# Kernel optimization log

Hardware: AMD Instinct MI355X
Metric: run time of the kernel (lower is better)

The kernel has to match this reference:

```python
import jax, jax.numpy as jnp
import numpy as np

# Config (scaled-down DeepSeek-style MoE)
B, S, H = 4, 1024, 1024       # batch, seq, hidden_size
I = 512                        # intermediate_size per expert
E = 64                         # num_routed_experts
K = 8                          # top-k
C = 1024
NS = 1                         # num_shared_experts


def setup_inputs() -> dict:
    key = jax.random.key(0)
    ks = jax.random.split(key, 8)
    def w(k, shape, fan_in):
        return jax.random.normal(k, shape, jnp.float32) / np.float32(np.sqrt(fan_in))
    return {
        "hidden_states": jax.random.normal(ks[0], (B, S, H), jnp.float32),
        "gate_w":    w(ks[1], (E, H), H),            # nn.Linear(H, E).weight
        "shared_wg": w(ks[2], (I * NS, H), H),       # shared SwiGLU gate_proj
        "shared_wu": w(ks[3], (I * NS, H), H),       # shared SwiGLU up_proj
        "shared_wd": w(ks[4], (H, I * NS), I * NS),  # shared SwiGLU down_proj
        "expert_wg": w(ks[5], (E, I, H), H),         # routed gate_proj, stacked
        "expert_wu": w(ks[6], (E, I, H), H),         # routed up_proj, stacked
        "expert_wd": w(ks[7], (E, H, I), I),         # routed down_proj, stacked
    }


def reference(hidden_states, gate_w, shared_wg, shared_wu, shared_wd,
              expert_wg, expert_wu, expert_wd):
    b, s, h = hidden_states.shape
    x = hidden_states.reshape(-1, h)                     # [T, H]
    T = x.shape[0]

    # ---- shared expert (SwiGLU) ----
    shared = (jax.nn.silu(x @ shared_wg.T) * (x @ shared_wu.T)) @ shared_wd.T

    # ---- gating: sigmoid scores, top-k, normalize by sum ----
    scores = jax.nn.sigmoid(x @ gate_w.T)                # [T, E]
    topw, topi = jax.lax.top_k(scores, K)                # [T, K]
    topw = topw / topw.sum(-1, keepdims=True)

    # ---- dispatch: position of each (token, slot) within its expert ----
    e_flat = topi.reshape(-1)                            # [N] expert id per routed row
    N = e_flat.shape[0]
    order = jnp.argsort(e_flat)                          # rows sorted by expert id
    sorted_e = e_flat[order]
    seg_start = jnp.searchsorted(sorted_e, jnp.arange(E))
    pos_sorted = (jnp.arange(N) - seg_start[sorted_e]).astype(jnp.int32)
    pos = jnp.zeros(N, jnp.int32).at[order].set(pos_sorted)  # slot within expert buffer

    tok = jnp.repeat(jnp.arange(T), K)                   # token id per routed row
    xin = x[tok]                                         # [N, H]

    # scatter tokens into per-expert buffers [E, C, H]
    buf = jnp.zeros((E, C, h), x.dtype).at[e_flat, pos].set(xin, mode='drop')

    # per-expert SwiGLU via batched GEMMs (grouped-GEMM equivalent)
    g = jax.nn.silu(jnp.einsum('ech,eih->eci', buf, expert_wg))
    u = jnp.einsum('ech,eih->eci', buf, expert_wu)
    out_buf = jnp.einsum('eci,ehi->ech', g * u, expert_wd)  # [E, C, H]

    # gather back and combine with normalized top-k weights
    rows = out_buf[e_flat, pos]                          # [N, H]
    routed = (rows.reshape(T, K, h) * topw[..., None]).sum(1)

    return (shared + routed).reshape(b, s, h)
```

## Files before the change

### kernel.cpp

```cpp
#include <hip/hip_runtime.h>
#include <hip/hip_bf16.h>

#define TOK 4096
#define HD 1024
#define ID 512
#define NE 64
#define TK 8
#define CAP 1024
#define NROUTE 32768
#define NCHUNK 128

typedef __attribute__((ext_vector_type(4))) float f32x4;
typedef __attribute__((ext_vector_type(8))) short s16x8;
typedef __attribute__((ext_vector_type(2))) __bf16 bf16x2;

__device__ __forceinline__ ushort f2bf(float f){
  uint u = __builtin_bit_cast(uint, f);
  u += 0x7fffu + ((u >> 16) & 1u);
  return (ushort)(u >> 16);
}
__device__ __forceinline__ float bf2f(ushort b){
  uint u = ((uint)b) << 16;
  return __builtin_bit_cast(float, u);
}
__device__ __forceinline__ uint2 f4_to_bf4(float4 v){
  bf16x2 p0; p0[0] = (__bf16)v.x; p0[1] = (__bf16)v.y;
  bf16x2 p1; p1[0] = (__bf16)v.z; p1[1] = (__bf16)v.w;
  uint2 r; r.x = __builtin_bit_cast(uint, p0); r.y = __builtin_bit_cast(uint, p1);
  return r;
}
__device__ __forceinline__ short bfs(float f){
  __bf16 h = (__bf16)f;
  return __builtin_bit_cast(short, h);
}
__device__ __forceinline__ s16x8 pack8(f32x4 a, f32x4 b){
  s16x8 r;
  r[0]=bfs(a[0]); r[1]=bfs(a[1]); r[2]=bfs(a[2]); r[3]=bfs(a[3]);
  r[4]=bfs(b[0]); r[5]=bfs(b[1]); r[6]=bfs(b[2]); r[7]=bfs(b[3]);
  return r;
}
__device__ __forceinline__ void gld16(void* lds, const void* g){
  __builtin_amdgcn_global_load_lds((const __attribute__((address_space(1))) unsigned int*)g,
                                   (__attribute__((address_space(3))) unsigned int*)lds, 16, 0, 0);
}

__global__ __launch_bounds__(256)
void cvtX_kernel(const float* __restrict__ X, ushort* __restrict__ Xbf){
  size_t i = ((size_t)blockIdx.x*256 + threadIdx.x) * 8;
  float4 a = *(const float4*)(X + i);
  float4 b = *(const float4*)(X + i + 4);
  uint2 lo = f4_to_bf4(a), hi = f4_to_bf4(b);
  uint4 o; o.x = lo.x; o.y = lo.y; o.z = hi.x; o.w = hi.y;
  *(uint4*)(Xbf + i) = o;
}

__global__ __launch_bounds__(256)
void gating_kernel(const float* __restrict__ X, const float* __restrict__ GW,
                   int* __restrict__ topi, float* __restrict__ topw)
{
  __shared__ float xt[16][68];
  __shared__ float gt[64][68];
  __shared__ double ds[16][72];
  const int tid = threadIdx.x;
  const int tbase = blockIdx.x * 16;
  const int t = tid & 15, e0 = (tid >> 4) * 4;
  double acc[4] = {0.0, 0.0, 0.0, 0.0};
  for (int hc=0; hc<HD; hc+=64){
    { int r = tid >> 4, c4 = (tid & 15) * 4;
      *(float4*)&xt[r][c4] = *(const float4*)(X + (size_t)(tbase+r)*HD + hc + c4); }
    #pragma unroll
    for (int it=0; it<4; ++it){
      int idx = it*256 + tid;
      int r = idx >> 4, c4 = (idx & 15) * 4;
      *(float4*)&gt[r][c4] = *(const float4*)(GW + (size_t)r*HD + hc + c4);
    }
    __syncthreads();
    #pragma unroll
    for (int k4=0; k4<16; ++k4){
      float4 xv = *(const float4*)&xt[t][k4*4];
      #pragma unroll
      for (int j=0;j<4;++j){
        float4 gv = *(const float4*)&gt[e0+j][k4*4];
        acc[j] += (double)xv.x*(double)gv.x + (double)xv.y*(double)gv.y
                + (double)xv.z*(double)gv.z + (double)xv.w*(double)gv.w;
      }
    }
    __syncthreads();
  }
  #pragma unroll
  for (int j=0;j<4;++j) ds[t][e0+j] = acc[j];
  __syncthreads();
  if (tid < 16){
    int tt = tid;
    int idxs[8]; double vals[8]; double sum = 0.0;
    #pragma unroll
    for (int k=0;k<8;++k){
      double best = -1e300; int bi = 0;
      for (int e=0;e<NE;++e){ double v = ds[tt][e]; if (v > best){ best = v; bi = e; } }
      ds[tt][bi] = -1e300;
      double w = 1.0 / (1.0 + exp(-best));
      idxs[k] = bi; vals[k] = w; sum += w;
    }
    double inv = 1.0 / sum;
    #pragma unroll
    for (int k=0;k<8;++k){
      topi[(size_t)(tbase+tt)*TK + k] = idxs[k];
      topw[(size_t)(tbase+tt)*TK + k] = (float)(vals[k]*inv);
    }
  }
}

__global__ __launch_bounds__(256)
void hist_kernel(const int* __restrict__ topi, int* __restrict__ ccnt){
  __shared__ int h[NE];
  const int tid = threadIdx.x;
  if (tid < NE) h[tid] = 0;
  __syncthreads();
  atomicAdd(&h[topi[blockIdx.x*256 + tid]], 1);
  __syncthreads();
  if (tid < NE) ccnt[blockIdx.x*NE + tid] = h[tid];
}

__global__ __launch_bounds__(64)
void scan_kernel(const int* __restrict__ ccnt, int* __restrict__ cbase,
                 int* __restrict__ cntC, int* __restrict__ ebase){
  const int e = threadIdx.x;
  int run = 0;
  for (int c=0;c<NCHUNK;++c){ cbase[c*NE+e] = run; run += ccnt[c*NE+e]; }
  cntC[e] = run < CAP ? run : CAP;
  __syncthreads();
  if (e == 0){
    int s = 0;
    for (int i=0;i<NE;++i){ ebase[i] = s; s += cntC[i]; }
    ebase[NE] = s;
  }
}

__global__ __launch_bounds__(64)
void assign_kernel(const int* __restrict__ topi, const int* __restrict__ cbase,
                   int* __restrict__ pos, int* __restrict__ rowlist){
  __shared__ int es[256];
  const int tid = threadIdx.x;
  const int c = blockIdx.x;
  for (int i=tid;i<256;i+=64) es[i] = topi[c*256+i];
  __syncthreads();
  const int e = tid;
  int cntr = cbase[c*NE+e];
  for (int j=0;j<256;++j){
    if (es[j] == e){
      int n = c*256+j;
      pos[n] = cntr;
      if (cntr < CAP) rowlist[e*CAP + cntr] = n;
      ++cntr;
    }
  }
}

template<bool SHARED>
__global__ __launch_bounds__(256,2)
void gateup_kernel(const ushort* __restrict__ Xbf, const float* __restrict__ WG,
                   const float* __restrict__ WU, const int* __restrict__ rowlist,
                   const int* __restrict__ cntC, const int* __restrict__ ebase,
                   ushort* __restrict__ interm)
{
  int e, mt, nt, cnt, outbase;
  if (SHARED){
    nt = blockIdx.x & 7; mt = blockIdx.x >> 3; e = 0; cnt = TOK; outbase = mt*128;
  } else {
    int x = blockIdx.x & 7; int rem = blockIdx.x >> 3;
    nt = rem & 7; mt = (rem >> 3) & 7; e = ((rem >> 6) << 3) | x;
    cnt = cntC[e];
    if (mt*128 >= cnt) return;
    outbase = ebase[e] + mt*128;
  }
  const size_t wof = SHARED ? 0 : (size_t)e*ID*HD;
  const float* wg = WG + wof + (size_t)nt*64*HD;
  const float* wu = WU + wof + (size_t)nt*64*HD;

  __shared__ ushort aL[64*128];
  __shared__ float  bF[128*64];
  __shared__ int tokb[128];

  const int tid = threadIdx.x;
  if (tid < 128){
    int tokv;
    if (SHARED) tokv = mt*128 + tid;
    else tokv = (mt*128 + tid < cnt) ? (rowlist[e*CAP + mt*128 + tid] >> 3) : 0;
    tokb[tid] = tokv;
  }
  __syncthreads();

  const int w = tid >> 6, l = tid & 63;
  const int wm = w >> 1, wn = w & 1;
  const int fr = l & 15, fko = (l >> 4) * 8;

  const ushort* aSrc[4];
  #pragma unroll
  for (int j=0;j<4;++j){
    int f = j*256 + tid;
    int L = f >> 4, s = f & 15;
    int g = s ^ (L & 15);
    int row = 2*L + (g >> 3);
    aSrc[j] = Xbf + (size_t)tokb[row]*HD + (g & 7)*8;
  }
  const float* bSrc[8];
  #pragma unroll
  for (int j=0;j<8;++j){
    int f = j*256 + tid;
    int R = f >> 4, s = f & 15;
    int g = s ^ (R & 15);
    const float* base = (j < 4) ? wg : wu;
    int r2 = (j < 4) ? R : (R - 64);
    bSrc[j] = base + (size_t)r2*HD + g*4;
  }

  f32x4 accg[4][2], accu[4][2];
  #pragma unroll
  for (int i=0;i<4;++i)
    #pragma unroll
    for (int j=0;j<2;++j){ accg[i][j] = (f32x4)0.0f; accu[i][j] = (f32x4)0.0f; }

  auto stage = [&](int kc){
    #pragma unroll
    for (int j=0;j<4;++j) gld16(aL + (size_t)(j*256 + w*64)*8, aSrc[j] + kc);
    #pragma unroll
    for (int j=0;j<8;++j) gld16(bF + (size_t)(j*256 + w*64)*4, bSrc[j] + kc);
  };

  stage(0);
  for (int kc=0; kc<HD; kc+=64){
    __syncthreads();
    #pragma unroll
    for (int ks=0; ks<2; ++ks){
      s16x8 a[4];
      #pragma unroll
      for (int mb=0; mb<4; ++mb){
        int r = wm*64 + mb*16 + fr;
        int agl = ks*4 + (fko >> 3);
        int g = ((r & 1) << 3) | agl;
        int L = r >> 1;
        int gs = g ^ (L & 15);
        a[mb] = *(const s16x8*)&aL[L*128 + gs*8];
      }
      #pragma unroll
      for (int cg=0; cg<2; ++cg){
        int Rg = wn*32 + cg*16 + fr;
        int gl0 = ks*8 + (fko >> 2);
        int x0 = Rg*64 + ((gl0 ^ (Rg & 15)) * 4);
        int x1 = Rg*64 + (((gl0+1) ^ (Rg & 15)) * 4);
        s16x8 bg = pack8(*(const f32x4*)&bF[x0], *(const f32x4*)&bF[x1]);
        int Ru = 64 + wn*32 + cg*16 + fr;
        int y0 = Ru*64 + ((gl0 ^ (Ru & 15)) * 4);
        int y1 = Ru*64 + (((gl0+1) ^ (Ru & 15)) * 4);
        s16x8 bu = pack8(*(const f32x4*)&bF[y0], *(const f32x4*)&bF[y1]);
        #pragma unroll
        for (int mb=0; mb<4; ++mb){
          accg[mb][cg] = __builtin_amdgcn_mfma_f32_16x16x32_bf16(a[mb], bg, accg[mb][cg], 0, 0, 0);
          accu[mb][cg] = __builtin_amdgcn_mfma_f32_16x16x32_bf16(a[mb], bu, accu[mb][cg], 0, 0, 0);
        }
      }
    }
    __syncthreads();
    if (kc + 64 < HD) stage(kc + 64);
  }

  const int rq = (l >> 4) * 4;
  #pragma unroll
  for (int mb=0; mb<4; ++mb){
    #pragma unroll
    for (int q=0; q<4; ++q){
      int rloc = wm*64 + mb*16 + rq + q;
      if (!SHARED && mt*128 + rloc >= cnt) continue;
      size_t orow = (size_t)(outbase + rloc);
      #pragma unroll
      for (int cg=0; cg<2; ++cg){
        float g = accg[mb][cg][q], u = accu[mb][cg][q];
        float sv = g / (1.0f + __expf(-g)) * u;
        interm[orow*ID + (size_t)(nt*64 + wn*32 + cg*16 + fr)] = f2bf(sv);
      }
    }
  }
}

template<bool SHARED>
__global__ __launch_bounds__(256,2)
void down_kernel(const ushort* __restrict__ interm, const float* __restrict__ WD,
                 const int* __restrict__ cntC, const int* __restrict__ ebase,
                 ushort* __restrict__ out_rows, float* __restrict__ outf)
{
  int e, mt, nt, cnt, abase;
  if (SHARED){
    nt = blockIdx.x & 7; mt = blockIdx.x >> 3; e = 0; cnt = TOK; abase = mt*128;
  } else {
    int x = blockIdx.x & 7; int rem = blockIdx.x >> 3;
    nt = rem & 7; mt = (rem >> 3) & 7; e = ((rem >> 6) << 3) | x;
    cnt = cntC[e];
    if (mt*128 >= cnt) return;
    abase = ebase[e] + mt*128;
  }
  const ushort* A = interm + (size_t)abase*ID;
  const float* wd = WD + (SHARED ? (size_t)0 : (size_t)e*HD*ID) + (size_t)nt*128*ID;

  __shared__ ushort aL[64*128];
  __shared__ float  bF[128*64];

  const int tid = threadIdx.x;
  const int w = tid >> 6, l = tid & 63;
  const int wm = w >> 1, wn = w & 1;
  const int fr = l & 15, fko = (l >> 4) * 8;

  const ushort* aSrc[4];
  #pragma unroll
  for (int j=0;j<4;++j){
    int f = j*256 + tid;
    int L = f >> 4, s = f & 15;
    int g = s ^ (L & 15);
    int row = 2*L + (g >> 3);
    aSrc[j] = A + (size_t)row*ID + (g & 7)*8;
  }
  const float* bSrc[8];
  #pragma unroll
  for (int j=0;j<8;++j){
    int f = j*256 + tid;
    int R = f >> 4, s = f & 15;
    int g = s ^ (R & 15);
    bSrc[j] = wd + (size_t)R*ID + g*4;
  }

  f32x4 acc[4][4];
  #pragma unroll
  for (int i=0;i<4;++i)
    #pragma unroll
    for (int j=0;j<4;++j) acc[i][j] = (f32x4)0.0f;

  auto stage = [&](int kc){
    #pragma unroll
    for (int j=0;j<4;++j) gld16(aL + (size_t)(j*256 + w*64)*8, aSrc[j] + kc);
    #pragma unroll
    for (int j=0;j<8;++j) gld16(bF + (size_t)(j*256 + w*64)*4, bSrc[j] + kc);
  };

  stage(0);
  for (int kc=0; kc<ID; kc+=64){
    __syncthreads();
    #pragma unroll
    for (int ks=0; ks<2; ++ks){
      s16x8 a[4];
      #pragma unroll
      for (int mb=0; mb<4; ++mb){
        int r = wm*64 + mb*16 + fr;
        int agl = ks*4 + (fko >> 3);
        int g = ((r & 1) << 3) | agl;
        int L = r >> 1;
        int gs = g ^ (L & 15);
        a[mb] = *(const s16x8*)&aL[L*128 + gs*8];
      }
      #pragma unroll
      for (int cg=0; cg<4; ++cg){
        int R = wn*64 + cg*16 + fr;
        int gl0 = ks*8 + (fko >> 2);
        int x0 = R*64 + ((gl0 ^ (R & 15)) * 4);
        int x1 = R*64 + (((gl0+1) ^ (R & 15)) * 4);
        s16x8 bd = pack8(*(const f32x4*)&bF[x0], *(const f32x4*)&bF[x1]);
        #pragma unroll
        for (int mb=0; mb<4; ++mb){
          acc[mb][cg] = __builtin_amdgcn_mfma_f32_16x16x32_bf16(a[mb], bd, acc[mb][cg], 0, 0, 0);
        }
      }
    }
    __syncthreads();
    if (kc + 64 < ID) stage(kc + 64);
  }

  const int rq = (l >> 4) * 4;
  #pragma unroll
  for (int mb=0; mb<4; ++mb){
    #pragma unroll
    for (int q=0; q<4; ++q){
      int rloc = wm*64 + mb*16 + rq + q;
      if (!SHARED && mt*128 + rloc >= cnt) continue;
      #pragma unroll
      for (int cg=0; cg<4; ++cg){
        float v = acc[mb][cg][q];
        int colg = nt*128 + wn*64 + cg*16 + fr;
        if (SHARED) outf[(size_t)(mt*128 + rloc)*HD + colg] = v;
        else        out_rows[(size_t)(abase + rloc)*HD + colg] = f2bf(v);
      }
    }
  }
}

__global__ __launch_bounds__(256)
void combine_kernel(const int* __restrict__ topi, const float* __restrict__ topw,
                    const int* __restrict__ pos, const int* __restrict__ ebase,
                    const ushort* __restrict__ out_rows, float* __restrict__ out)
{
  const int t = blockIdx.x;
  const int tid = threadIdx.x;
  __shared__ int rws[TK];
  __shared__ float wts[TK];
  if (tid < TK){
    int e = topi[(size_t)t*TK + tid];
    int p = pos[(size_t)t*TK + tid];
    rws[tid] = (p < CAP) ? (ebase[e] + p) : -1;
    wts[tid] = topw[(size_t)t*TK + tid];
  }
  __syncthreads();
  const int h0 = tid * 4;
  float4 acc = *(float4*)(out + (size_t)t*HD + h0);
  #pragma unroll
  for (int k=0;k<TK;++k){
    int r = rws[k];
    if (r < 0) continue;
    ushort4 v = *(const ushort4*)(out_rows + (size_t)r*HD + h0);
    float wk = wts[k];
    acc.x += wk*bf2f(v.x); acc.y += wk*bf2f(v.y);
    acc.z += wk*bf2f(v.z); acc.w += wk*bf2f(v.w);
  }
  *(float4*)(out + (size_t)t*HD + h0) = acc;
}

extern "C" void kernel_launch(void* const* d_in, const int* in_sizes, int n_in,
                              void* d_out, int out_size, void* d_ws, size_t ws_size,
                              hipStream_t stream)
{
  (void)in_sizes; (void)n_in; (void)out_size; (void)ws_size;
  const float* X   = (const float*)d_in[0];
  const float* GW  = (const float*)d_in[1];
  const float* SWG = (const float*)d_in[2];
  const float* SWU = (const float*)d_in[3];
  const float* SWD = (const float*)d_in[4];
  const float* EWG = (const float*)d_in[5];
  const float* EWU = (const float*)d_in[6];
  const float* EWD = (const float*)d_in[7];
  float* OUT = (float*)d_out;

  char* p = (char*)d_ws;
  int*    topi    = (int*)p;      p += (size_t)NROUTE*4;
  float*  topw    = (float*)p;    p += (size_t)NROUTE*4;
  int*    pos     = (int*)p;      p += (size_t)NROUTE*4;
  int*    ccnt    = (int*)p;      p += (size_t)NCHUNK*NE*4;
  int*    cbase   = (int*)p;      p += (size_t)NCHUNK*NE*4;
  int*    cntC    = (int*)p;      p += 256;
  int*    ebase   = (int*)p;      p += 512;
  int*    rowlist = (int*)p;      p += (size_t)NE*CAP*4;
  ushort* Xbf     = (ushort*)p;   p += (size_t)TOK*HD*2;
  ushort* interm_r= (ushort*)p;   p += (size_t)(NROUTE+128)*ID*2;
  ushort* interm_s= (ushort*)p;   p += (size_t)TOK*ID*2;
  ushort* out_rows= (ushort*)p;   p += (size_t)NROUTE*HD*2;

  cvtX_kernel<<<TOK*HD/8/256, 256, 0, stream>>>(X, Xbf);
  gating_kernel<<<256, 256, 0, stream>>>(X, GW, topi, topw);
  hist_kernel<<<NCHUNK, 256, 0, stream>>>(topi, ccnt);
  scan_kernel<<<1, 64, 0, stream>>>(ccnt, cbase, cntC, ebase);
  assign_kernel<<<NCHUNK, 64, 0, stream>>>(topi, cbase, pos, rowlist);

  gateup_kernel<false><<<4096, 256, 0, stream>>>(Xbf, EWG, EWU, rowlist, cntC, ebase, interm_r);
  gateup_kernel<true ><<<256,  256, 0, stream>>>(Xbf, SWG, SWU, nullptr, nullptr, nullptr, interm_s);
  down_kernel<false><<<4096, 256, 0, stream>>>(interm_r, EWD, cntC, ebase, out_rows, nullptr);
  down_kernel<true ><<<256,  256, 0, stream>>>(interm_s, SWD, nullptr, nullptr, nullptr, OUT);

  combine_kernel<<<TOK, 256, 0, stream>>>(topi, topw, pos, ebase, out_rows, OUT);
}
```

Baseline: 391.6 us.

## Use 32x32x16 MFMA with 256-row tiles and fragment-ordered LDS layout

Both expert GEMM kernels switch from 16x16x32 to 32x32x16 bf16 MFMA. The M tile grows from 128 to 256 rows per block, which halves the grid and the number of times the fp32 weights are re-read per expert. The LDS layout is reorganized so each lane's MFMA fragment is stored contiguously, replacing the XOR swizzle. The risks are more wasted work on partially filled 256-row expert tiles, fewer blocks in flight, higher accumulator register pressure, and possible LDS bank conflicts on the staging writes.

Result: slower. 577.5 us (+47.5%).

```diff
diff --git a/kernel.cpp b/kernel.cpp
--- a/kernel.cpp
+++ b/kernel.cpp
@@ -11,6 +11,7 @@
 #define NCHUNK 128
 
 typedef __attribute__((ext_vector_type(4))) float f32x4;
+typedef __attribute__((ext_vector_type(16))) float f32x16;
 typedef __attribute__((ext_vector_type(8))) short s16x8;
 typedef __attribute__((ext_vector_type(2))) __bf16 bf16x2;
 
@@ -165,64 +166,59 @@
 {
   int e, mt, nt, cnt, outbase;
   if (SHARED){
-    nt = blockIdx.x & 7; mt = blockIdx.x >> 3; e = 0; cnt = TOK; outbase = mt*128;
+    nt = blockIdx.x & 7; mt = blockIdx.x >> 3; e = 0; cnt = TOK; outbase = mt*256;
   } else {
     int x = blockIdx.x & 7; int rem = blockIdx.x >> 3;
-    nt = rem & 7; mt = (rem >> 3) & 7; e = ((rem >> 6) << 3) | x;
+    nt = rem & 7; mt = (rem >> 3) & 3; e = ((rem >> 5) << 3) | x;
     cnt = cntC[e];
-    if (mt*128 >= cnt) return;
-    outbase = ebase[e] + mt*128;
+    if (mt*256 >= cnt) return;
+    outbase = ebase[e] + mt*256;
   }
   const size_t wof = SHARED ? 0 : (size_t)e*ID*HD;
   const float* wg = WG + wof + (size_t)nt*64*HD;
   const float* wu = WU + wof + (size_t)nt*64*HD;
 
-  __shared__ ushort aL[64*128];
-  __shared__ float  bF[128*64];
-  __shared__ int tokb[128];
-
-  const int tid = threadIdx.x;
-  if (tid < 128){
+  __shared__ ushort aL[32*64*8];
+  __shared__ float  bF[32*64*4];
+  __shared__ int tokb[256];
+
+  const int tid = threadIdx.x;
+  {
     int tokv;
-    if (SHARED) tokv = mt*128 + tid;
-    else tokv = (mt*128 + tid < cnt) ? (rowlist[e*CAP + mt*128 + tid] >> 3) : 0;
+    if (SHARED) tokv = mt*256 + tid;
+    else tokv = (mt*256 + tid < cnt) ? (rowlist[e*CAP + mt*256 + tid] >> 3) : 0;
     tokb[tid] = tokv;
   }
   __syncthreads();
 
   const int w = tid >> 6, l = tid & 63;
   const int wm = w >> 1, wn = w & 1;
-  const int fr = l & 15, fko = (l >> 4) * 8;
-
-  const ushort* aSrc[4];
-  #pragma unroll
-  for (int j=0;j<4;++j){
-    int f = j*256 + tid;
-    int L = f >> 4, s = f & 15;
-    int g = s ^ (L & 15);
-    int row = 2*L + (g >> 3);
-    aSrc[j] = Xbf + (size_t)tokb[row]*HD + (g & 7)*8;
+  const int lr = l & 31, lk = (l >> 5) * 8;
+
+  const ushort* aSrc[8];
+  #pragma unroll
+  for (int j=0;j<8;++j){
+    int G = j*4 + w;
+    int ks = G >> 3, rb = G & 7;
+    aSrc[j] = Xbf + (size_t)tokb[rb*32 + lr]*HD + ks*16 + lk;
   }
   const float* bSrc[8];
   #pragma unroll
   for (int j=0;j<8;++j){
-    int f = j*256 + tid;
-    int R = f >> 4, s = f & 15;
-    int g = s ^ (R & 15);
-    const float* base = (j < 4) ? wg : wu;
-    int r2 = (j < 4) ? R : (R - 64);
-    bSrc[j] = base + (size_t)r2*HD + g*4;
-  }
-
-  f32x4 accg[4][2], accu[4][2];
-  #pragma unroll
-  for (int i=0;i<4;++i)
-    #pragma unroll
-    for (int j=0;j<2;++j){ accg[i][j] = (f32x4)0.0f; accu[i][j] = (f32x4)0.0f; }
+    int G = j*4 + w;
+    int half = G & 1, q = G >> 1;
+    int wnb = q & 1, mat = (q >> 1) & 1, ks = q >> 2;
+    const float* base = mat ? wu : wg;
+    bSrc[j] = base + (size_t)(wnb*32 + lr)*HD + ks*16 + lk + half*4;
+  }
+
+  f32x16 accg[4], accu[4];
+  #pragma unroll
+  for (int i=0;i<4;++i){ accg[i] = (f32x16)0.0f; accu[i] = (f32x16)0.0f; }
 
   auto stage = [&](int kc){
     #pragma unroll
-    for (int j=0;j<4;++j) gld16(aL + (size_t)(j*256 + w*64)*8, aSrc[j] + kc);
+    for (int j=0;j<8;++j) gld16(aL + (size_t)(j*256 + w*64)*8, aSrc[j] + kc);
     #pragma unroll
     for (int j=0;j<8;++j) gld16(bF + (size_t)(j*256 + w*64)*4, bSrc[j] + kc);
   };
@@ -231,53 +227,39 @@
   for (int kc=0; kc<HD; kc+=64){
     __syncthreads();
     #pragma unroll
-    for (int ks=0; ks<2; ++ks){
+    for (int ks=0; ks<4; ++ks){
       s16x8 a[4];
       #pragma unroll
-      for (int mb=0; mb<4; ++mb){
-        int r = wm*64 + mb*16 + fr;
-        int agl = ks*4 + (fko >> 3);
-        int g = ((r & 1) << 3) | agl;
-        int L = r >> 1;
-        int gs = g ^ (L & 15);
-        a[mb] = *(const s16x8*)&aL[L*128 + gs*8];
-      }
-      #pragma unroll
-      for (int cg=0; cg<2; ++cg){
-        int Rg = wn*32 + cg*16 + fr;
-        int gl0 = ks*8 + (fko >> 2);
-        int x0 = Rg*64 + ((gl0 ^ (Rg & 15)) * 4);
-        int x1 = Rg*64 + (((gl0+1) ^ (Rg & 15)) * 4);
-        s16x8 bg = pack8(*(const f32x4*)&bF[x0], *(const f32x4*)&bF[x1]);
-        int Ru = 64 + wn*32 + cg*16 + fr;
-        int y0 = Ru*64 + ((gl0 ^ (Ru & 15)) * 4);
-        int y1 = Ru*64 + (((gl0+1) ^ (Ru & 15)) * 4);
-        s16x8 bu = pack8(*(const f32x4*)&bF[y0], *(const f32x4*)&bF[y1]);
-        #pragma unroll
-        for (int mb=0; mb<4; ++mb){
-          accg[mb][cg] = __builtin_amdgcn_mfma_f32_16x16x32_bf16(a[mb], bg, accg[mb][cg], 0, 0, 0);
-          accu[mb][cg] = __builtin_amdgcn_mfma_f32_16x16x32_bf16(a[mb], bu, accu[mb][cg], 0, 0, 0);
-        }
+      for (int rb=0; rb<4; ++rb){
+        int G = ks*8 + wm*4 + rb;
+        a[rb] = *(const s16x8*)&aL[(G*64 + l)*8];
+      }
+      int qg = ks*4 + wn;
+      int qu = ks*4 + 2 + wn;
+      s16x8 bg = pack8(*(const f32x4*)&bF[(qg*2*64 + l)*4],
+                       *(const f32x4*)&bF[((qg*2+1)*64 + l)*4]);
+      s16x8 bu = pack8(*(const f32x4*)&bF[(qu*2*64 + l)*4],
+                       *(const f32x4*)&bF[((qu*2+1)*64 + l)*4]);
+      #pragma unroll
+      for (int rb=0; rb<4; ++rb){
+        accg[rb] = __builtin_amdgcn_mfma_f32_32x32x16_bf16(a[rb], bg, accg[rb], 0, 0, 0);
+        accu[rb] = __builtin_amdgcn_mfma_f32_32x32x16_bf16(a[rb], bu, accu[rb], 0, 0, 0);
       }
     }
     __syncthreads();
     if (kc + 64 < HD) stage(kc + 64);
   }
 
-  const int rq = (l >> 4) * 4;
-  #pragma unroll
-  for (int mb=0; mb<4; ++mb){
-    #pragma unroll
-    for (int q=0; q<4; ++q){
-      int rloc = wm*64 + mb*16 + rq + q;
-      if (!SHARED && mt*128 + rloc >= cnt) continue;
-      size_t orow = (size_t)(outbase + rloc);
-      #pragma unroll
-      for (int cg=0; cg<2; ++cg){
-        float g = accg[mb][cg][q], u = accu[mb][cg][q];
-        float sv = g / (1.0f + __expf(-g)) * u;
-        interm[orow*ID + (size_t)(nt*64 + wn*32 + cg*16 + fr)] = f2bf(sv);
-      }
+  #pragma unroll
+  for (int rb=0; rb<4; ++rb){
+    #pragma unroll
+    for (int r=0; r<16; ++r){
+      int rowl = (r & 3) + 8*(r >> 2) + 4*(l >> 5);
+      int rloc = wm*128 + rb*32 + rowl;
+      if (!SHARED && mt*256 + rloc >= cnt) continue;
+      float g = accg[rb][r], u = accu[rb][r];
+      float sv = g / (1.0f + __expf(-g)) * u;
+      interm[(size_t)(outbase + rloc)*ID + nt*64 + wn*32 + lr] = f2bf(sv);
     }
   }
 }
@@ -290,52 +272,50 @@
 {
   int e, mt, nt, cnt, abase;
   if (SHARED){
-    nt = blockIdx.x & 7; mt = blockIdx.x >> 3; e = 0; cnt = TOK; abase = mt*128;
+    nt = blockIdx.x & 7; mt = blockIdx.x >> 3; e = 0; cnt = TOK; abase = mt*256;
   } else {
     int x = blockIdx.x & 7; int rem = blockIdx.x >> 3;
-    nt = rem & 7; mt = (rem >> 3) & 7; e = ((rem >> 6) << 3) | x;
+    nt = rem & 7; mt = (rem >> 3) & 3; e = ((rem >> 5) << 3) | x;
     cnt = cntC[e];
-    if (mt*128 >= cnt) return;
-    abase = ebase[e] + mt*128;
+    if (mt*256 >= cnt) return;
+    abase = ebase[e] + mt*256;
   }
   const ushort* A = interm + (size_t)abase*ID;
   const float* wd = WD + (SHARED ? (size_t)0 : (size_t)e*HD*ID) + (size_t)nt*128*ID;
 
-  __shared__ ushort aL[64*128];
-  __shared__ float  bF[128*64];
+  __shared__ ushort aL[32*64*8];
+  __shared__ float  bF[32*64*4];
 
   const int tid = threadIdx.x;
   const int w = tid >> 6, l = tid & 63;
   const int wm = w >> 1, wn = w & 1;
-  const int fr = l & 15, fko = (l >> 4) * 8;
-
-  const ushort* aSrc[4];
-  #pragma unroll
-  for (int j=0;j<4;++j){
-    int f = j*256 + tid;
-    int L = f >> 4, s = f & 15;
-    int g = s ^ (L & 15);
-    int row = 2*L + (g >> 3);
-    aSrc[j] = A + (size_t)row*ID + (g & 7)*8;
+  const int lr = l & 31, lk = (l >> 5) * 8;
+
+  const ushort* aSrc[8];
+  #pragma unroll
+  for (int j=0;j<8;++j){
+    int G = j*4 + w;
+    int ks = G >> 3, rb = G & 7;
+    aSrc[j] = A + (size_t)(rb*32 + lr)*ID + ks*16 + lk;
   }
   const float* bSrc[8];
   #pragma unroll
   for (int j=0;j<8;++j){
-    int f = j*256 + tid;
-    int R = f >> 4, s = f & 15;
-    int g = s ^ (R & 15);
-    bSrc[j] = wd + (size_t)R*ID + g*4;
-  }
-
-  f32x4 acc[4][4];
+    int G = j*4 + w;
+    int half = G & 1, q = G >> 1;
+    int cf = q & 3, ks = q >> 2;
+    bSrc[j] = wd + (size_t)(cf*32 + lr)*ID + ks*16 + lk + half*4;
+  }
+
+  f32x16 acc[4][2];
   #pragma unroll
   for (int i=0;i<4;++i)
     #pragma unroll
-    for (int j=0;j<4;++j) acc[i][j] = (f32x4)0.0f;
+    for (int jx=0;jx<2;++jx) acc[i][jx] = (f32x16)0.0f;
 
   auto stage = [&](int kc){
     #pragma unroll
-    for (int j=0;j<4;++j) gld16(aL + (size_t)(j*256 + w*64)*8, aSrc[j] + kc);
+    for (int j=0;j<8;++j) gld16(aL + (size_t)(j*256 + w*64)*8, aSrc[j] + kc);
     #pragma unroll
     for (int j=0;j<8;++j) gld16(bF + (size_t)(j*256 + w*64)*4, bSrc[j] + kc);
   };
@@ -344,46 +324,39 @@
   for (int kc=0; kc<ID; kc+=64){
     __syncthreads();
     #pragma unroll
-    for (int ks=0; ks<2; ++ks){
+    for (int ks=0; ks<4; ++ks){
       s16x8 a[4];
       #pragma unroll
-      for (int mb=0; mb<4; ++mb){
-        int r = wm*64 + mb*16 + fr;
-        int agl = ks*4 + (fko >> 3);
-        int g = ((r & 1) << 3) | agl;
-        int L = r >> 1;
-        int gs = g ^ (L & 15);
-        a[mb] = *(const s16x8*)&aL[L*128 + gs*8];
-      }
-      #pragma unroll
-      for (int cg=0; cg<4; ++cg){
-        int R = wn*64 + cg*16 + fr;
-        int gl0 = ks*8 + (fko >> 2);
-        int x0 = R*64 + ((gl0 ^ (R & 15)) * 4);
-        int x1 = R*64 + (((gl0+1) ^ (R & 15)) * 4);
-        s16x8 bd = pack8(*(const f32x4*)&bF[x0], *(const f32x4*)&bF[x1]);
+      for (int rb=0; rb<4; ++rb){
+        int G = ks*8 + wm*4 + rb;
+        a[rb] = *(const s16x8*)&aL[(G*64 + l)*8];
+      }
+      #pragma unroll
+      for (int cg=0; cg<2; ++cg){
+        int q = ks*4 + wn*2 + cg;
+        s16x8 bd = pack8(*(const f32x4*)&bF[(q*2*64 + l)*4],
+                         *(const f32x4*)&bF[((q*2+1)*64 + l)*4]);
         #pragma unroll
-        for (int mb=0; mb<4; ++mb){
-          acc[mb][cg] = __builtin_amdgcn_mfma_f32_16x16x32_bf16(a[mb], bd, acc[mb][cg], 0, 0, 0);
-        }
+        for (int rb=0; rb<4; ++rb)
+          acc[rb][cg] = __builtin_amdgcn_mfma_f32_32x32x16_bf16(a[rb], bd, acc[rb][cg], 0, 0, 0);
       }
     }
     __syncthreads();
     if (kc + 64 < ID) stage(kc + 64);
   }
 
-  const int rq = (l >> 4) * 4;
-  #pragma unroll
-  for (int mb=0; mb<4; ++mb){
-    #pragma unroll
-    for (int q=0; q<4; ++q){
-      int rloc = wm*64 + mb*16 + rq + q;
-      if (!SHARED && mt*128 + rloc >= cnt) continue;
-      #pragma unroll
-      for (int cg=0; cg<4; ++cg){
-        float v = acc[mb][cg][q];
-        int colg = nt*128 + wn*64 + cg*16 + fr;
-        if (SHARED) outf[(size_t)(mt*128 + rloc)*HD + colg] = v;
+  #pragma unroll
+  for (int rb=0; rb<4; ++rb){
+    #pragma unroll
+    for (int cg=0; cg<2; ++cg){
+      #pragma unroll
+      for (int r=0; r<16; ++r){
+        int rowl = (r & 3) + 8*(r >> 2) + 4*(l >> 5);
+        int rloc = wm*128 + rb*32 + rowl;
+        if (!SHARED && mt*256 + rloc >= cnt) continue;
+        float v = acc[rb][cg][r];
+        int colg = nt*128 + wn*64 + cg*32 + lr;
+        if (SHARED) outf[(size_t)(mt*256 + rloc)*HD + colg] = v;
         else        out_rows[(size_t)(abase + rloc)*HD + colg] = f2bf(v);
       }
     }
@@ -445,7 +418,7 @@
   int*    ebase   = (int*)p;      p += 512;
   int*    rowlist = (int*)p;      p += (size_t)NE*CAP*4;
   ushort* Xbf     = (ushort*)p;   p += (size_t)TOK*HD*2;
-  ushort* interm_r= (ushort*)p;   p += (size_t)(NROUTE+128)*ID*2;
+  ushort* interm_r= (ushort*)p;   p += (size_t)(NROUTE+256)*ID*2;
   ushort* interm_s= (ushort*)p;   p += (size_t)TOK*ID*2;
   ushort* out_rows= (ushort*)p;   p += (size_t)NROUTE*HD*2;
 
@@ -455,10 +428,10 @@
   scan_kernel<<<1, 64, 0, stream>>>(ccnt, cbase, cntC, ebase);
   assign_kernel<<<NCHUNK, 64, 0, stream>>>(topi, cbase, pos, rowlist);
 
-  gateup_kernel<false><<<4096, 256, 0, stream>>>(Xbf, EWG, EWU, rowlist, cntC, ebase, interm_r);
-  gateup_kernel<true ><<<256,  256, 0, stream>>>(Xbf, SWG, SWU, nullptr, nullptr, nullptr, interm_s);
-  down_kernel<false><<<4096, 256, 0, stream>>>(interm_r, EWD, cntC, ebase, out_rows, nullptr);
-  down_kernel<true ><<<256,  256, 0, stream>>>(interm_s, SWD, nullptr, nullptr, nullptr, OUT);
+  gateup_kernel<false><<<2048, 256, 0, stream>>>(Xbf, EWG, EWU, rowlist, cntC, ebase, interm_r);
+  gateup_kernel<true ><<<128,  256, 0, stream>>>(Xbf, SWG, SWU, nullptr, nullptr, nullptr, interm_s);
+  down_kernel<false><<<2048, 256, 0, stream>>>(interm_r, EWD, cntC, ebase, out_rows, nullptr);
+  down_kernel<true ><<<128,  256, 0, stream>>>(interm_s, SWD, nullptr, nullptr, nullptr, OUT);
 
   combine_kernel<<<TOK, 256, 0, stream>>>(topi, topw, pos, ebase, out_rows, OUT);
 }
```

## Convert fp32 weights to bf16 at LDS staging with register prefetch

Applied to the files above, without the earlier changes.

Both the gate/up and down GEMM kernels now load fp32 weight tiles into registers, convert them to bf16 once, and store them to a swizzled bf16 LDS tile. Previously the fp32 tiles went straight to LDS and were re-converted by every wave on each fragment read. The next tile's weights are prefetched into registers during the MFMA loop. This halves the LDS footprint and traffic for B and removes the redundant conversions. In exchange it adds registers, replaces async global-to-LDS loads with synchronous loads, and adds a second barrier per iteration.

Result: slower. 436.9 us (+11.6%).

```diff
diff --git a/kernel.cpp b/kernel.cpp
--- a/kernel.cpp
+++ b/kernel.cpp
@@ -33,10 +33,10 @@
   __bf16 h = (__bf16)f;
   return __builtin_bit_cast(short, h);
 }
-__device__ __forceinline__ s16x8 pack8(f32x4 a, f32x4 b){
+__device__ __forceinline__ s16x8 pack8(float4 a, float4 b){
   s16x8 r;
-  r[0]=bfs(a[0]); r[1]=bfs(a[1]); r[2]=bfs(a[2]); r[3]=bfs(a[3]);
-  r[4]=bfs(b[0]); r[5]=bfs(b[1]); r[6]=bfs(b[2]); r[7]=bfs(b[3]);
+  r[0]=bfs(a.x); r[1]=bfs(a.y); r[2]=bfs(a.z); r[3]=bfs(a.w);
+  r[4]=bfs(b.x); r[5]=bfs(b.y); r[6]=bfs(b.z); r[7]=bfs(b.w);
   return r;
 }
 __device__ __forceinline__ void gld16(void* lds, const void* g){
@@ -178,7 +178,7 @@
   const float* wu = WU + wof + (size_t)nt*64*HD;
 
   __shared__ ushort aL[64*128];
-  __shared__ float  bF[128*64];
+  __shared__ ushort bB[64*128];
   __shared__ int tokb[128];
 
   const int tid = threadIdx.x;
@@ -203,15 +203,16 @@
     int row = 2*L + (g >> 3);
     aSrc[j] = Xbf + (size_t)tokb[row]*HD + (g & 7)*8;
   }
-  const float* bSrc[8];
-  #pragma unroll
-  for (int j=0;j<8;++j){
-    int f = j*256 + tid;
-    int R = f >> 4, s = f & 15;
-    int g = s ^ (R & 15);
-    const float* base = (j < 4) ? wg : wu;
-    int r2 = (j < 4) ? R : (R - 64);
-    bSrc[j] = base + (size_t)r2*HD + g*4;
+  const float* bSrc[4]; int bDst[4];
+  #pragma unroll
+  for (int i=0;i<4;++i){
+    int f = i*256 + tid;
+    int L = f >> 4, s = f & 15;
+    int g = s ^ (L & 15);
+    int brow = 2*L + (g >> 3);
+    int gk = g & 7;
+    bSrc[i] = ((brow < 64) ? (wg + (size_t)brow*HD) : (wu + (size_t)(brow-64)*HD)) + gk*8;
+    bDst[i] = f*8;
   }
 
   f32x4 accg[4][2], accu[4][2];
@@ -220,39 +221,48 @@
     #pragma unroll
     for (int j=0;j<2;++j){ accg[i][j] = (f32x4)0.0f; accu[i][j] = (f32x4)0.0f; }
 
-  auto stage = [&](int kc){
+  float4 brv[8];
+  auto loadB = [&](int kc){
+    #pragma unroll
+    for (int i=0;i<4;++i){
+      brv[2*i]   = *(const float4*)(bSrc[i] + kc);
+      brv[2*i+1] = *(const float4*)(bSrc[i] + kc + 4);
+    }
+  };
+  auto writeB = [&](){
+    #pragma unroll
+    for (int i=0;i<4;++i) *(s16x8*)&bB[bDst[i]] = pack8(brv[2*i], brv[2*i+1]);
+  };
+  auto stageA = [&](int kc){
     #pragma unroll
     for (int j=0;j<4;++j) gld16(aL + (size_t)(j*256 + w*64)*8, aSrc[j] + kc);
-    #pragma unroll
-    for (int j=0;j<8;++j) gld16(bF + (size_t)(j*256 + w*64)*4, bSrc[j] + kc);
-  };
-
-  stage(0);
-  for (int kc=0; kc<HD; kc+=64){
-    __syncthreads();
+  };
+
+  loadB(0); stageA(0); writeB();
+  __syncthreads();
+
+  for (int t=0; t<16; ++t){
+    const int kc = t*64;
+    if (t < 15) loadB(kc + 64);
     #pragma unroll
     for (int ks=0; ks<2; ++ks){
+      int gk = ks*4 + (fko >> 3);
       s16x8 a[4];
       #pragma unroll
       for (int mb=0; mb<4; ++mb){
         int r = wm*64 + mb*16 + fr;
-        int agl = ks*4 + (fko >> 3);
-        int g = ((r & 1) << 3) | agl;
+        int g = ((r & 1) << 3) | gk;
         int L = r >> 1;
-        int gs = g ^ (L & 15);
-        a[mb] = *(const s16x8*)&aL[L*128 + gs*8];
+        a[mb] = *(const s16x8*)&aL[L*128 + ((g ^ (L & 15)))*8];
       }
       #pragma unroll
       for (int cg=0; cg<2; ++cg){
         int Rg = wn*32 + cg*16 + fr;
-        int gl0 = ks*8 + (fko >> 2);
-        int x0 = Rg*64 + ((gl0 ^ (Rg & 15)) * 4);
-        int x1 = Rg*64 + (((gl0+1) ^ (Rg & 15)) * 4);
-        s16x8 bg = pack8(*(const f32x4*)&bF[x0], *(const f32x4*)&bF[x1]);
+        int Lg = Rg >> 1, gg = ((Rg & 1) << 3) | gk;
+        s16x8 bg = *(const s16x8*)&bB[Lg*128 + ((gg ^ (Lg & 15)))*8];
         int Ru = 64 + wn*32 + cg*16 + fr;
-        int y0 = Ru*64 + ((gl0 ^ (Ru & 15)) * 4);
-        int y1 = Ru*64 + (((gl0+1) ^ (Ru & 15)) * 4);
-        s16x8 bu = pack8(*(const f32x4*)&bF[y0], *(const f32x4*)&bF[y1]);
+        int Lu = Ru >> 1, gu = ((Ru & 1) << 3) | gk;
+        s16x8 bu = *(const s16x8*)&bB[Lu*128 + ((gu ^ (Lu & 15)))*8];
         #pragma unroll
         for (int mb=0; mb<4; ++mb){
           accg[mb][cg] = __builtin_amdgcn_mfma_f32_16x16x32_bf16(a[mb], bg, accg[mb][cg], 0, 0, 0);
@@ -261,7 +271,8 @@
       }
     }
     __syncthreads();
-    if (kc + 64 < HD) stage(kc + 64);
+    if (t < 15){ writeB(); stageA(kc + 64); }
+    __syncthreads();
   }
 
   const int rq = (l >> 4) * 4;
@@ -302,7 +313,7 @@
   const float* wd = WD + (SHARED ? (size_t)0 : (size_t)e*HD*ID) + (size_t)nt*128*ID;
 
   __shared__ ushort aL[64*128];
-  __shared__ float  bF[128*64];
+  __shared__ ushort bB[64*128];
 
   const int tid = threadIdx.x;
   const int w = tid >> 6, l = tid & 63;
@@ -318,13 +329,16 @@
     int row = 2*L + (g >> 3);
     aSrc[j] = A + (size_t)row*ID + (g & 7)*8;
   }
-  const float* bSrc[8];
-  #pragma unroll
-  for (int j=0;j<8;++j){
-    int f = j*256 + tid;
-    int R = f >> 4, s = f & 15;
-    int g = s ^ (R & 15);
-    bSrc[j] = wd + (size_t)R*ID + g*4;
+  const float* bSrc[4]; int bDst[4];
+  #pragma unroll
+  for (int i=0;i<4;++i){
+    int f = i*256 + tid;
+    int L = f >> 4, s = f & 15;
+    int g = s ^ (L & 15);
+    int brow = 2*L + (g >> 3);
+    int gk = g & 7;
+    bSrc[i] = wd + (size_t)brow*ID + gk*8;
+    bDst[i] = f*8;
   }
 
   f32x4 acc[4][4];
@@ -333,35 +347,45 @@
     #pragma unroll
     for (int j=0;j<4;++j) acc[i][j] = (f32x4)0.0f;
 
-  auto stage = [&](int kc){
+  float4 brv[8];
+  auto loadB = [&](int kc){
+    #pragma unroll
+    for (int i=0;i<4;++i){
+      brv[2*i]   = *(const float4*)(bSrc[i] + kc);
+      brv[2*i+1] = *(const float4*)(bSrc[i] + kc + 4);
+    }
+  };
+  auto writeB = [&](){
+    #pragma unroll
+    for (int i=0;i<4;++i) *(s16x8*)&bB[bDst[i]] = pack8(brv[2*i], brv[2*i+1]);
+  };
+  auto stageA = [&](int kc){
     #pragma unroll
     for (int j=0;j<4;++j) gld16(aL + (size_t)(j*256 + w*64)*8, aSrc[j] + kc);
-    #pragma unroll
-    for (int j=0;j<8;++j) gld16(bF + (size_t)(j*256 + w*64)*4, bSrc[j] + kc);
-  };
-
-  stage(0);
-  for (int kc=0; kc<ID; kc+=64){
-    __syncthreads();
+  };
+
+  loadB(0); stageA(0); writeB();
+  __syncthreads();
+
+  for (int t=0; t<8; ++t){
+    const int kc = t*64;
+    if (t < 7) loadB(kc + 64);
     #pragma unroll
     for (int ks=0; ks<2; ++ks){
+      int gk = ks*4 + (fko >> 3);
       s16x8 a[4];
       #pragma unroll
       for (int mb=0; mb<4; ++mb){
         int r = wm*64 + mb*16 + fr;
-        int agl = ks*4 + (fko >> 3);
-        int g = ((r & 1) << 3) | agl;
+        int g = ((r & 1) << 3) | gk;
         int L = r >> 1;
-        int gs = g ^ (L & 15);
-        a[mb] = *(const s16x8*)&aL[L*128 + gs*8];
+        a[mb] = *(const s16x8*)&aL[L*128 + ((g ^ (L & 15)))*8];
       }
       #pragma unroll
       for (int cg=0; cg<4; ++cg){
         int R = wn*64 + cg*16 + fr;
-        int gl0 = ks*8 + (fko >> 2);
-        int x0 = R*64 + ((gl0 ^ (R & 15)) * 4);
-        int x1 = R*64 + (((gl0+1) ^ (R & 15)) * 4);
-        s16x8 bd = pack8(*(const f32x4*)&bF[x0], *(const f32x4*)&bF[x1]);
+        int L = R >> 1, g = ((R & 1) << 3) | gk;
+        s16x8 bd = *(const s16x8*)&bB[L*128 + ((g ^ (L & 15)))*8];
         #pragma unroll
         for (int mb=0; mb<4; ++mb){
           acc[mb][cg] = __builtin_amdgcn_mfma_f32_16x16x32_bf16(a[mb], bd, acc[mb][cg], 0, 0, 0);
@@ -369,7 +393,8 @@
       }
     }
     __syncthreads();
-    if (kc + 64 < ID) stage(kc + 64);
+    if (t < 7){ writeB(); stageA(kc + 64); }
+    __syncthreads();
   }
 
   const int rq = (l >> 4) * 4;
```

## Fuse X bf16 conversion into gating and merge shared/routed GEMM launches

Applied to the files above, without the earlier changes.

Folds the fp32-to-bf16 conversion of X into the gating kernel, which already reads X, so one full pass over the input and one launch go away. The shared-expert gate/up and down GEMMs are merged into the routed-expert launches as extra blocks selected by block index. This removes two more launches and lets shared-expert work fill in behind the tail of routed blocks. In exchange, the template specialisation becomes a runtime branch, which may add register pressure and divergent setup.

New measurement: 361.5 us (median of 2 runs). -7.7%, faster.

```diff
diff --git a/kernel.cpp b/kernel.cpp
--- a/kernel.cpp
+++ b/kernel.cpp
@@ -45,17 +45,8 @@
 }
 
 __global__ __launch_bounds__(256)
-void cvtX_kernel(const float* __restrict__ X, ushort* __restrict__ Xbf){
-  size_t i = ((size_t)blockIdx.x*256 + threadIdx.x) * 8;
-  float4 a = *(const float4*)(X + i);
-  float4 b = *(const float4*)(X + i + 4);
-  uint2 lo = f4_to_bf4(a), hi = f4_to_bf4(b);
-  uint4 o; o.x = lo.x; o.y = lo.y; o.z = hi.x; o.w = hi.y;
-  *(uint4*)(Xbf + i) = o;
-}
-
-__global__ __launch_bounds__(256)
 void gating_kernel(const float* __restrict__ X, const float* __restrict__ GW,
+                   ushort* __restrict__ Xbf,
                    int* __restrict__ topi, float* __restrict__ topw)
 {
   __shared__ float xt[16][68];
@@ -67,7 +58,10 @@
   double acc[4] = {0.0, 0.0, 0.0, 0.0};
   for (int hc=0; hc<HD; hc+=64){
     { int r = tid >> 4, c4 = (tid & 15) * 4;
-      *(float4*)&xt[r][c4] = *(const float4*)(X + (size_t)(tbase+r)*HD + hc + c4); }
+      float4 v = *(const float4*)(X + (size_t)(tbase+r)*HD + hc + c4);
+      *(float4*)&xt[r][c4] = v;
+      *(uint2*)(Xbf + (size_t)(tbase+r)*HD + hc + c4) = f4_to_bf4(v);
+    }
     #pragma unroll
     for (int it=0; it<4; ++it){
       int idx = it*256 + tid;
@@ -156,26 +150,34 @@
   }
 }
 
-template<bool SHARED>
 __global__ __launch_bounds__(256,2)
-void gateup_kernel(const ushort* __restrict__ Xbf, const float* __restrict__ WG,
-                   const float* __restrict__ WU, const int* __restrict__ rowlist,
-                   const int* __restrict__ cntC, const int* __restrict__ ebase,
-                   ushort* __restrict__ interm)
+void gateup_kernel(const ushort* __restrict__ Xbf,
+                   const float* __restrict__ WG, const float* __restrict__ WU,
+                   const float* __restrict__ SWG, const float* __restrict__ SWU,
+                   const int* __restrict__ rowlist, const int* __restrict__ cntC,
+                   const int* __restrict__ ebase,
+                   ushort* __restrict__ interm_r, ushort* __restrict__ interm_s)
 {
-  int e, mt, nt, cnt, outbase;
-  if (SHARED){
-    nt = blockIdx.x & 7; mt = blockIdx.x >> 3; e = 0; cnt = TOK; outbase = mt*128;
+  int nt, mt, cnt, outbase;
+  const float *wg, *wu;
+  ushort* interm;
+  const bool shared_p = (blockIdx.x >= 4096u);
+  const int e_rl = shared_p ? 0 : ((((blockIdx.x >> 3) >> 6) << 3) | (blockIdx.x & 7));
+  if (shared_p){
+    int b = blockIdx.x - 4096;
+    nt = b & 7; mt = b >> 3; cnt = TOK; outbase = mt*128;
+    wg = SWG + (size_t)nt*64*HD; wu = SWU + (size_t)nt*64*HD;
+    interm = interm_s;
   } else {
-    int x = blockIdx.x & 7; int rem = blockIdx.x >> 3;
-    nt = rem & 7; mt = (rem >> 3) & 7; e = ((rem >> 6) << 3) | x;
-    cnt = cntC[e];
+    int rem = blockIdx.x >> 3;
+    nt = rem & 7; mt = (rem >> 3) & 7;
+    cnt = cntC[e_rl];
     if (mt*128 >= cnt) return;
-    outbase = ebase[e] + mt*128;
-  }
-  const size_t wof = SHARED ? 0 : (size_t)e*ID*HD;
-  const float* wg = WG + wof + (size_t)nt*64*HD;
-  const float* wu = WU + wof + (size_t)nt*64*HD;
+    outbase = ebase[e_rl] + mt*128;
+    const size_t wof = (size_t)e_rl*ID*HD;
+    wg = WG + wof + (size_t)nt*64*HD; wu = WU + wof + (size_t)nt*64*HD;
+    interm = interm_r;
+  }
 
   __shared__ ushort aL[64*128];
   __shared__ float  bF[128*64];
@@ -184,8 +186,8 @@
   const int tid = threadIdx.x;
   if (tid < 128){
     int tokv;
-    if (SHARED) tokv = mt*128 + tid;
-    else tokv = (mt*128 + tid < cnt) ? (rowlist[e*CAP + mt*128 + tid] >> 3) : 0;
+    if (shared_p) tokv = mt*128 + tid;
+    else tokv = (mt*128 + tid < cnt) ? (rowlist[e_rl*CAP + mt*128 + tid] >> 3) : 0;
     tokb[tid] = tokv;
   }
   __syncthreads();
@@ -270,7 +272,7 @@
     #pragma unroll
     for (int q=0; q<4; ++q){
       int rloc = wm*64 + mb*16 + rq + q;
-      if (!SHARED && mt*128 + rloc >= cnt) continue;
+      if (mt*128 + rloc >= cnt) continue;
       size_t orow = (size_t)(outbase + rloc);
       #pragma unroll
       for (int cg=0; cg<2; ++cg){
@@ -282,24 +284,30 @@
   }
 }
 
-template<bool SHARED>
 __global__ __launch_bounds__(256,2)
-void down_kernel(const ushort* __restrict__ interm, const float* __restrict__ WD,
+void down_kernel(const ushort* __restrict__ interm_r, const ushort* __restrict__ interm_s,
+                 const float* __restrict__ WD, const float* __restrict__ SWD,
                  const int* __restrict__ cntC, const int* __restrict__ ebase,
                  ushort* __restrict__ out_rows, float* __restrict__ outf)
 {
-  int e, mt, nt, cnt, abase;
-  if (SHARED){
-    nt = blockIdx.x & 7; mt = blockIdx.x >> 3; e = 0; cnt = TOK; abase = mt*128;
+  int nt, mt, cnt, abase;
+  const ushort* A;
+  const float* wd;
+  const bool shared_p = (blockIdx.x >= 4096u);
+  if (shared_p){
+    int b = blockIdx.x - 4096;
+    nt = b & 7; mt = b >> 3; cnt = TOK; abase = mt*128;
+    A = interm_s + (size_t)abase*ID;
+    wd = SWD + (size_t)nt*128*ID;
   } else {
     int x = blockIdx.x & 7; int rem = blockIdx.x >> 3;
-    nt = rem & 7; mt = (rem >> 3) & 7; e = ((rem >> 6) << 3) | x;
+    nt = rem & 7; mt = (rem >> 3) & 7; int e = ((rem >> 6) << 3) | x;
     cnt = cntC[e];
     if (mt*128 >= cnt) return;
     abase = ebase[e] + mt*128;
-  }
-  const ushort* A = interm + (size_t)abase*ID;
-  const float* wd = WD + (SHARED ? (size_t)0 : (size_t)e*HD*ID) + (size_t)nt*128*ID;
+    A = interm_r + (size_t)abase*ID;
+    wd = WD + (size_t)e*HD*ID + (size_t)nt*128*ID;
+  }
 
   __shared__ ushort aL[64*128];
   __shared__ float  bF[128*64];
@@ -378,13 +386,13 @@
     #pragma unroll
     for (int q=0; q<4; ++q){
       int rloc = wm*64 + mb*16 + rq + q;
-      if (!SHARED && mt*128 + rloc >= cnt) continue;
+      if (mt*128 + rloc >= cnt) continue;
       #pragma unroll
       for (int cg=0; cg<4; ++cg){
         float v = acc[mb][cg][q];
         int colg = nt*128 + wn*64 + cg*16 + fr;
-        if (SHARED) outf[(size_t)(mt*128 + rloc)*HD + colg] = v;
-        else        out_rows[(size_t)(abase + rloc)*HD + colg] = f2bf(v);
+        if (shared_p) outf[(size_t)(mt*128 + rloc)*HD + colg] = v;
+        else          out_rows[(size_t)(abase + rloc)*HD + colg] = f2bf(v);
       }
     }
   }
@@ -449,16 +457,15 @@
   ushort* interm_s= (ushort*)p;   p += (size_t)TOK*ID*2;
   ushort* out_rows= (ushort*)p;   p += (size_t)NROUTE*HD*2;
 
-  cvtX_kernel<<<TOK*HD/8/256, 256, 0, stream>>>(X, Xbf);
-  gating_kernel<<<256, 256, 0, stream>>>(X, GW, topi, topw);
+  gating_kernel<<<256, 256, 0, stream>>>(X, GW, Xbf, topi, topw);
   hist_kernel<<<NCHUNK, 256, 0, stream>>>(topi, ccnt);
   scan_kernel<<<1, 64, 0, stream>>>(ccnt, cbase, cntC, ebase);
   assign_kernel<<<NCHUNK, 64, 0, stream>>>(topi, cbase, pos, rowlist);
 
-  gateup_kernel<false><<<4096, 256, 0, stream>>>(Xbf, EWG, EWU, rowlist, cntC, ebase, interm_r);
-  gateup_kernel<true ><<<256,  256, 0, stream>>>(Xbf, SWG, SWU, nullptr, nullptr, nullptr, interm_s);
-  down_kernel<false><<<4096, 256, 0, stream>>>(interm_r, EWD, cntC, ebase, out_rows, nullptr);
-  down_kernel<true ><<<256,  256, 0, stream>>>(interm_s, SWD, nullptr, nullptr, nullptr, OUT);
+  gateup_kernel<<<4352, 256, 0, stream>>>(Xbf, EWG, EWU, SWG, SWU,
+                                          rowlist, cntC, ebase, interm_r, interm_s);
+  down_kernel<<<4352, 256, 0, stream>>>(interm_r, interm_s, EWD, SWD,
+                                        cntC, ebase, out_rows, OUT);
 
   combine_kernel<<<TOK, 256, 0, stream>>>(topi, topw, pos, ebase, out_rows, OUT);
 }
```
